# Kernel tuning notes

Measured on AMD Instinct MI355X. Metric: run time of the kernel, lower is better.

## Reference

```python
import jax, jax.numpy as jnp
import numpy as np

N_NODES = 50000
N_EDGES = 800000
N_GRAPHS = 256
F_IN = 112   # num_features
DIM = 32     # hidden dim of 2nd GIN layer
OUT_DIM = 64 # output_dim
BN_EPS = 1e-5


def setup_inputs() -> dict:
    key = jax.random.key(0)
    ks = jax.random.split(key, 20)
    def w(k, shape, s=0.05):
        return jax.random.normal(k, shape, dtype=jnp.float32) * s
    return {
        "x": jax.random.normal(ks[0], (N_NODES, F_IN), dtype=jnp.float32),
        "src": jax.random.randint(ks[1], (N_EDGES,), 0, N_NODES),
        "dst": jax.random.randint(ks[2], (N_EDGES,), 0, N_NODES),
        "batch": jnp.sort(jax.random.randint(ks[3], (N_NODES,), 0, N_GRAPHS)),
        # GIN layer 1 MLP: Linear(112,112) -> ReLU -> Linear(112,112)
        "g1_w1": w(ks[4], (F_IN, F_IN)), "g1_b1": jnp.zeros((F_IN,), jnp.float32),
        "g1_w2": w(ks[5], (F_IN, F_IN)), "g1_b2": jnp.zeros((F_IN,), jnp.float32),
        "bn1_g": jnp.ones((F_IN,), jnp.float32), "bn1_b": jnp.zeros((F_IN,), jnp.float32),
        # GIN layer 2 MLP: Linear(112,32) -> ReLU -> Linear(32,32)
        "g2_w1": w(ks[6], (F_IN, DIM)), "g2_b1": jnp.zeros((DIM,), jnp.float32),
        "g2_w2": w(ks[7], (DIM, DIM)), "g2_b2": jnp.zeros((DIM,), jnp.float32),
        "bn2_g": jnp.ones((DIM,), jnp.float32), "bn2_b": jnp.zeros((DIM,), jnp.float32),
        # graph-level head
        "fcxd_w": w(ks[8], (DIM, OUT_DIM)), "fcxd_b": jnp.zeros((OUT_DIM,), jnp.float32),
        "fc1_w": w(ks[9], (64, 32)), "fc1_b": jnp.zeros((32,), jnp.float32),
        "fc2_w": w(ks[10], (32, 16)), "fc2_b": jnp.zeros((16,), jnp.float32),
        "fc3_w": w(ks[11], (16, 8)), "fc3_b": jnp.zeros((8,), jnp.float32),
        "fc4_w": w(ks[12], (8, 2)), "fc4_b": jnp.zeros((2,), jnp.float32),
        "fc5_w": w(ks[13], (2, 1)), "fc5_b": jnp.zeros((1,), jnp.float32),
    }


def _batchnorm(h, g, b):
    # training-mode BatchNorm1d: batch statistics over node axis
    m = h.mean(axis=0)
    v = h.var(axis=0)
    return (h - m) * jax.lax.rsqrt(v + BN_EPS) * g + b


def reference(x, src, dst, batch,
              g1_w1, g1_b1, g1_w2, g1_b2, bn1_g, bn1_b,
              g2_w1, g2_b1, g2_w2, g2_b2, bn2_g, bn2_b,
              fcxd_w, fcxd_b, fc1_w, fc1_b, fc2_w, fc2_b,
              fc3_w, fc3_b, fc4_w, fc4_b, fc5_w, fc5_b):
    # --- GIN layer 1: agg = sum_{j in N(i)} x_j ; h = MLP(x + agg) (eps=0) ---
    agg = jax.ops.segment_sum(x[src], dst, num_segments=N_NODES)
    h = x + agg
    h = jnp.maximum(h @ g1_w1 + g1_b1, 0.0) @ g1_w2 + g1_b2
    h = jnp.maximum(h, 0.0)                     # F.relu after conv
    h = _batchnorm(h, bn1_g, bn1_b)
    # --- GIN layer 2 ---
    agg = jax.ops.segment_sum(h[src], dst, num_segments=N_NODES)
    h = h + agg
    h = jnp.maximum(h @ g2_w1 + g2_b1, 0.0) @ g2_w2 + g2_b2
    h = jnp.maximum(h, 0.0)
    h = _batchnorm(h, bn2_g, bn2_b)
    # --- global_add_pool over graph ids ---
    pooled = jax.ops.segment_sum(h, batch, num_segments=N_GRAPHS)  # [G, 32]
    z = jnp.maximum(pooled @ fcxd_w + fcxd_b, 0.0)  # dropout = identity (eval)
    # dense head: NO activations between fc1..fc5 in the original code
    z = z @ fc1_w + fc1_b
    z = z @ fc2_w + fc2_b
    z = z @ fc3_w + fc3_b
    z = z @ fc4_w + fc4_b
    z = z @ fc5_w + fc5_b
    return z  # [N_GRAPHS, 1]
```

## Files before the change

kernel.cpp:

```cpp
#include <hip/hip_runtime.h>
#include <hip/hip_fp16.h>

#define N_NODES 50000
#define N_GRAPHS 256
#define N_EDGES 800000
#define F_IN 112
#define DIM 32
#define BN_EPS 1e-5
#define HROW 128
#define CAP 64
#define CB 391
#define CBCAP 2560
#define CHUNK 8192
#define NPART 98
#define GEMM_MB 782
#define WS 40

typedef __attribute__((ext_vector_type(8))) _Float16 half8;
typedef __attribute__((ext_vector_type(4))) float float4v;

__device__ inline unsigned short f2h_u(float f) {
    union { __half h; unsigned short u; } v; v.h = __float2half(f); return v.u;
}
__device__ inline float h2f_u(unsigned short u) {
    union { unsigned short u; __half h; } v; v.u = u; return __half2float(v.h);
}

__device__ inline void acc8(const uint4& u, float* ax) {
    const __half2* h = (const __half2*)&u;
#pragma unroll
    for (int p = 0; p < 4; p++) {
        float2 f = __half22float2(h[p]);
        ax[2 * p] += f.x;
        ax[2 * p + 1] += f.y;
    }
}

__device__ inline void w_split_body(const float* __restrict__ W, int K, int N, int Kpad,
                                    unsigned short* __restrict__ hi_t,
                                    unsigned short* __restrict__ lo_t, int idx) {
    if (idx >= N * Kpad) return;
    int n = idx / Kpad, k = idx - n * Kpad;
    float v = (k < K) ? W[(size_t)k * N + n] : 0.f;
    unsigned short h = f2h_u(v);
    hi_t[idx] = h;
    lo_t[idx] = f2h_u(v - h2f_u(h));
}

#define MB_P  NPART
#define MB_XH (MB_P + 3126)
#define MB_W1 (MB_XH + 14)
#define MB_W2 (MB_W1 + 14)
#define MB_W4 (MB_W2 + 1)
#define MB_GB (MB_W4 + 49)
__global__ __launch_bounds__(1024) void build_kernel(
        const int* __restrict__ src, const int* __restrict__ dst,
        int* __restrict__ gcur,
        int* __restrict__ bucket,
        const float* __restrict__ X, __half* __restrict__ Xh,
        const float* __restrict__ g1_w1, unsigned short* w1h, unsigned short* w1l,
        const float* __restrict__ g1_w2, unsigned short* w2h, unsigned short* w2l,
        const float* __restrict__ g2_w2, unsigned short* w4h, unsigned short* w4l,
        const int* __restrict__ batch, int* __restrict__ goff) {
    int b = blockIdx.x;
    int t = threadIdx.x;
    if (b < MB_P) {
        __shared__ int hist[512];
        __shared__ int lofs[512];
        __shared__ int lcur[512];
        __shared__ int gbase[512];
        __shared__ int staging[CHUNK];
        int base = b * CHUNK;
        int total = min(CHUNK, N_EDGES - base);
        for (int i = t; i < 512; i += 1024) hist[i] = 0;
        __syncthreads();
        int d[8], s[8];
#pragma unroll
        for (int j = 0; j < 8; j++) {
            int i = base + j * 1024 + t;
            if (i < N_EDGES) {
                d[j] = __builtin_nontemporal_load(dst + i);
                s[j] = __builtin_nontemporal_load(src + i);
            } else {
                d[j] = -1;
            }
        }
#pragma unroll
        for (int j = 0; j < 8; j++) {
            if (d[j] >= 0) atomicAdd(&hist[d[j] >> 7], 1);
        }
        __syncthreads();
        if (t < 512) lofs[t] = hist[t];
        __syncthreads();
        for (int o = 1; o < 512; o <<= 1) {
            int add = (t < 512 && t >= o) ? lofs[t - o] : 0;
            __syncthreads();
            if (t < 512) lofs[t] += add;
            __syncthreads();
        }
        if (t < CB) {
            gbase[t] = (hist[t] > 0) ? atomicAdd(&gcur[t], hist[t]) : 0;
        }
        if (t < 512) lcur[t] = lofs[t] - hist[t];
        __syncthreads();
#pragma unroll
        for (int j = 0; j < 8; j++) {
            if (d[j] >= 0) {
                int bb = d[j] >> 7;
                int p = atomicAdd(&lcur[bb], 1);
                staging[p] = (d[j] << 16) | s[j];
            }
        }
        __syncthreads();
        for (int p = t; p < total; p += 1024) {
            int e = staging[p];
            int bb = ((unsigned)e >> 16) >> 7;
            int ls = lofs[bb] - hist[bb];
            int di = gbase[bb] + (p - ls);
            if (di < CBCAP) bucket[(size_t)bb * CBCAP + di] = e;
        }
    } else if (b < MB_XH) {
        int idx = (b - MB_P) * 1024 + t;
        if (idx >= (N_NODES + 1) * (HROW / 2)) return;
        int row = idx >> 6, c2 = idx & 63;
        int col = c2 * 2;
        float2 v = make_float2(0.f, 0.f);
        if (row < N_NODES && col < F_IN) v = *(const float2*)(X + (size_t)row * F_IN + col);
        ((__half2*)Xh)[idx] = __floats2half2_rn(v.x, v.y);
    } else if (b < MB_W1) {
        w_split_body(g1_w1, F_IN, F_IN, 128, w1h, w1l, (b - MB_XH) * 1024 + t);
    } else if (b < MB_W2) {
        w_split_body(g1_w2, F_IN, F_IN, 128, w2h, w2l, (b - MB_W1) * 1024 + t);
    } else if (b < MB_W4) {
        w_split_body(g2_w2, DIM, DIM, 32, w4h, w4l, (b - MB_W2) * 1024 + t);
    } else {
        int i = (b - MB_W4) * 1024 + t;
        if (i >= N_NODES) return;
        int cur = batch[i];
        int prev = (i == 0) ? -1 : batch[i - 1];
        for (int g = prev + 1; g <= cur; g++) goff[g] = i;
        if (i == N_NODES - 1) {
            for (int g = cur + 1; g <= N_GRAPHS; g++) goff[g] = N_NODES;
        }
    }
}

__global__ __launch_bounds__(1024) void bin_build(const int* __restrict__ gcur,
                                                  const int* __restrict__ bucket,
                                                  unsigned short* __restrict__ perm_pad,
                                                  int* __restrict__ deg) {
    __shared__ __align__(16) unsigned short bins[128][CAP];
    __shared__ int lcur[128];
    int b = blockIdx.x, t = threadIdx.x;
    for (int i = t; i < 128 * CAP; i += 1024) ((unsigned short*)bins)[i] = (unsigned short)N_NODES;
    if (t < 128) lcur[t] = 0;
    __syncthreads();
    int count = min(gcur[b], CBCAP);
    for (int i = t; i < count; i += 1024) {
        int e = bucket[(size_t)b * CBCAP + i];
        int l = ((unsigned)e >> 16) & 127;
        int s = e & 0xFFFF;
        int c = atomicAdd(&lcur[l], 1);
        if (c < CAP) bins[l][c] = (unsigned short)s;
    }
    __syncthreads();
    if (t < 128) {
        int node = b * 128 + t;
        if (node < N_NODES) deg[node] = min(lcur[t], CAP);
    }
    for (int i = t; i < 128 * (CAP / 8); i += 1024) {
        int l = i >> 3, q = i & 7;
        int node = b * 128 + l;
        if (node < N_NODES) {
            ((int4*)&perm_pad[(size_t)node * CAP])[q] = ((const int4*)bins[l])[q];
        }
    }
}

__global__ __launch_bounds__(1024, 8) void gin1_fused(const float* __restrict__ X,
        const __half* __restrict__ Xh,
        const int* __restrict__ deg_arr,
        const unsigned short* __restrict__ perm_pad,
        const unsigned short* __restrict__ W1h, const unsigned short* __restrict__ W1l,
        const float* __restrict__ b1,
        const unsigned short* __restrict__ W2h, const unsigned short* __restrict__ W2l,
        const float* __restrict__ b2,
        __half* __restrict__ Ch, float* __restrict__ pbuf, int M) {
    constexpr int N = 112, Kpad = 128, TS = 136, AS = 136;
    __shared__ __align__(16) unsigned short Afull[64 * AS];
    __shared__ __align__(16) unsigned short T1[64 * TS];
    __shared__ __align__(16) unsigned short Wh[N * WS];
    __shared__ __align__(16) unsigned short Wl[N * WS];
    float* sls = (float*)Afull;
    int t = threadIdx.x;
    int lane = t & 63, wid = t >> 6;
    int r0 = blockIdx.x * 64;
    int m = lane & 15, quad = lane >> 4;
    int rg = wid & 3, ng = wid >> 2;
    int nt0 = ng, nt1 = ng + 4;
    bool has1 = (nt1 < 7);

    for (int idx = t; idx < N * 8; idx += 1024) {
        int n = idx >> 3, w = idx & 7;
        int gsrc = n * (Kpad / 4) + w;
        ((uint2*)&Wh[n * WS])[w] = ((const uint2*)W1h)[gsrc];
        ((uint2*)&Wl[n * WS])[w] = ((const uint2*)W1l)[gsrc];
    }

    int fl = lane & 15, eg = lane >> 4;
#pragma unroll 1
    for (int i = 0; i < 4; i++) {
        int row = wid * 4 + i;
        int grow = r0 + row;
        float ax[8] = {0.f, 0.f, 0.f, 0.f, 0.f, 0.f, 0.f, 0.f};
        if (grow < M) {
            int deg = deg_arr[grow];
            const unsigned short* pl = perm_pad + (size_t)grow * CAP;
            int nb = (deg + 3) >> 2;
#pragma unroll 1
            for (int b = 0; b < nb; b += 4) {
                int s0 = pl[(b + 0) * 4 + eg];
                int s1 = pl[(b + 1) * 4 + eg];
                int s2 = pl[(b + 2) * 4 + eg];
                int s3 = pl[(b + 3) * 4 + eg];
                uint4 u0 = *(const uint4*)(Xh + (size_t)s0 * HROW + fl * 8);
                uint4 u1 = *(const uint4*)(Xh + (size_t)s1 * HROW + fl * 8);
                uint4 u2 = *(const uint4*)(Xh + (size_t)s2 * HROW + fl * 8);
                uint4 u3 = *(const uint4*)(Xh + (size_t)s3 * HROW + fl * 8);
                acc8(u0, ax); acc8(u1, ax); acc8(u2, ax); acc8(u3, ax);
            }
        }
#pragma unroll
        for (int p = 0; p < 8; p++) {
            ax[p] += __shfl_xor(ax[p], 16);
            ax[p] += __shfl_xor(ax[p], 32);
        }
        if (eg == 0) {
            if (grow < M && fl < 14) {
                float4 sa = *(const float4*)(X + (size_t)grow * F_IN + fl * 8);
                float4 sb = *(const float4*)(X + (size_t)grow * F_IN + fl * 8 + 4);
                ax[0] += sa.x; ax[1] += sa.y; ax[2] += sa.z; ax[3] += sa.w;
                ax[4] += sb.x; ax[5] += sb.y; ax[6] += sb.z; ax[7] += sb.w;
            }
            uint4 o;
            __half2* oh = (__half2*)&o;
#pragma unroll
            for (int p = 0; p < 4; p++) oh[p] = __floats2half2_rn(ax[2 * p], ax[2 * p + 1]);
            *(uint4*)&Afull[row * AS + fl * 8] = o;
        }
    }
    {
        int i = t;
        T1[(i >> 4) * TS + 112 + (i & 15)] = 0;
    }

    float4v acc0 = {0.f, 0.f, 0.f, 0.f}, acc1 = {0.f, 0.f, 0.f, 0.f};

    for (int c = 0; c < 4; c++) {
        int kc = c * 32;
        if (c > 0) {
            for (int idx = t; idx < N * 8; idx += 1024) {
                int n = idx >> 3, w = idx & 7;
                int gsrc = n * (Kpad / 4) + (kc >> 2) + w;
                ((uint2*)&Wh[n * WS])[w] = ((const uint2*)W1h)[gsrc];
                ((uint2*)&Wl[n * WS])[w] = ((const uint2*)W1l)[gsrc];
            }
        }
        __syncthreads();
        half8 a = *(const half8*)&Afull[(rg * 16 + m) * AS + kc + quad * 8];
        {
            half8 bh = *(const half8*)&Wh[(nt0 * 16 + m) * WS + quad * 8];
            half8 bl = *(const half8*)&Wl[(nt0 * 16 + m) * WS + quad * 8];
            acc0 = __builtin_amdgcn_mfma_f32_16x16x32_f16(a, bh, acc0, 0, 0, 0);
            acc0 = __builtin_amdgcn_mfma_f32_16x16x32_f16(a, bl, acc0, 0, 0, 0);
        }
        if (has1) {
            half8 bh = *(const half8*)&Wh[(nt1 * 16 + m) * WS + quad * 8];
            half8 bl = *(const half8*)&Wl[(nt1 * 16 + m) * WS + quad * 8];
            acc1 = __builtin_amdgcn_mfma_f32_16x16x32_f16(a, bh, acc1, 0, 0, 0);
            acc1 = __builtin_amdgcn_mfma_f32_16x16x32_f16(a, bl, acc1, 0, 0, 0);
        }
        __syncthreads();
    }

    {
        int col = nt0 * 16 + m;
        float bb = b1[col];
#pragma unroll
        for (int r = 0; r < 4; r++)
            T1[(rg * 16 + quad * 4 + r) * TS + col] = f2h_u(fmaxf(acc0[r] + bb, 0.f));
        acc0 = (float4v){0.f, 0.f, 0.f, 0.f};
    }
    if (has1) {
        int col = nt1 * 16 + m;
        float bb = b1[col];
#pragma unroll
        for (int r = 0; r < 4; r++)
            T1[(rg * 16 + quad * 4 + r) * TS + col] = f2h_u(fmaxf(acc1[r] + bb, 0.f));
        acc1 = (float4v){0.f, 0.f, 0.f, 0.f};
    }
    __syncthreads();

    for (int c = 0; c < 4; c++) {
        int kc = c * 32;
        for (int idx = t; idx < N * 8; idx += 1024) {
            int n = idx >> 3, w = idx & 7;
            int gsrc = n * (Kpad / 4) + (kc >> 2) + w;
            ((uint2*)&Wh[n * WS])[w] = ((const uint2*)W2h)[gsrc];
            ((uint2*)&Wl[n * WS])[w] = ((const uint2*)W2l)[gsrc];
        }
        __syncthreads();
        half8 a = *(const half8*)&T1[(rg * 16 + m) * TS + kc + quad * 8];
        {
            half8 bh = *(const half8*)&Wh[(nt0 * 16 + m) * WS + quad * 8];
            half8 bl = *(const half8*)&Wl[(nt0 * 16 + m) * WS + quad * 8];
            acc0 = __builtin_amdgcn_mfma_f32_16x16x32_f16(a, bh, acc0, 0, 0, 0);
            acc0 = __builtin_amdgcn_mfma_f32_16x16x32_f16(a, bl, acc0, 0, 0, 0);
        }
        if (has1) {
            half8 bh = *(const half8*)&Wh[(nt1 * 16 + m) * WS + quad * 8];
            half8 bl = *(const half8*)&Wl[(nt1 * 16 + m) * WS + quad * 8];
            acc1 = __builtin_amdgcn_mfma_f32_16x16x32_f16(a, bh, acc1, 0, 0, 0);
            acc1 = __builtin_amdgcn_mfma_f32_16x16x32_f16(a, bl, acc1, 0, 0, 0);
        }
        __syncthreads();
    }

    float st_s0 = 0.f, st_q0 = 0.f, st_s1 = 0.f, st_q1 = 0.f;
    {
        int col = nt0 * 16 + m;
        float bb = b2[col];
#pragma unroll
        for (int r = 0; r < 4; r++) {
            int row = r0 + rg * 16 + quad * 4 + r;
            float v = fmaxf(acc0[r] + bb, 0.f);
            if (row < M) {
                Ch[(size_t)row * HROW + col] = __float2half(v);
                st_s0 += v;
                st_q0 += v * v;
            }
        }
    }
    if (has1) {
        int col = nt1 * 16 + m;
        float bb = b2[col];
#pragma unroll
        for (int r = 0; r < 4; r++) {
            int row = r0 + rg * 16 + quad * 4 + r;
            float v = fmaxf(acc1[r] + bb, 0.f);
            if (row < M) {
                Ch[(size_t)row * HROW + col] = __float2half(v);
                st_s1 += v;
                st_q1 += v * v;
            }
        }
    }
    if (t < 128) {
        int row = r0 + (t >> 1), o = (t & 1) * 8;
        if (row < M) *(uint4*)((unsigned short*)Ch + (size_t)row * HROW + 112 + o) = make_uint4(0, 0, 0, 0);
    }
    st_s0 += __shfl_xor(st_s0, 16); st_s0 += __shfl_xor(st_s0, 32);
    st_q0 += __shfl_xor(st_q0, 16); st_q0 += __shfl_xor(st_q0, 32);
    st_s1 += __shfl_xor(st_s1, 16); st_s1 += __shfl_xor(st_s1, 32);
    st_q1 += __shfl_xor(st_q1, 16); st_q1 += __shfl_xor(st_q1, 32);
    if (quad == 0) {
        sls[rg * 2 * N + nt0 * 16 + m] = st_s0;
        sls[rg * 2 * N + N + nt0 * 16 + m] = st_q0;
        if (has1) {
            sls[rg * 2 * N + nt1 * 16 + m] = st_s1;
            sls[rg * 2 * N + N + nt1 * 16 + m] = st_q1;
        }
    }
    __syncthreads();
    if (t < 2 * N) {
        pbuf[(size_t)blockIdx.x * 2 * N + t] = sls[0 * 2 * N + t] + sls[1 * 2 * N + t] +
                                               sls[2 * 2 * N + t] + sls[3 * 2 * N + t];
    }
}

__global__ __launch_bounds__(256) void bn1_w3(const float* __restrict__ pbuf,
                                              const float* __restrict__ gg,
                                              const float* __restrict__ bb,
                                              const float* __restrict__ W,
                                              unsigned short* __restrict__ w3h,
                                              unsigned short* __restrict__ w3l,
                                              float* __restrict__ c0,
                                              __half* __restrict__ ysent, int M) {
    __shared__ double red[256];
    __shared__ float sv[2];
    int j = blockIdx.x;
    int t = threadIdx.x;
    if (j == 0 && t >= 64 && t < 96) ysent[t - 64] = __float2half(0.f);
    double sum = 0.0, sq = 0.0;
    for (int i = t; i < GEMM_MB; i += 256) {
        sum += (double)pbuf[(size_t)i * 2 * F_IN + j];
        sq  += (double)pbuf[(size_t)i * 2 * F_IN + F_IN + j];
    }
    red[t] = sum;
    __syncthreads();
    for (int o = 128; o > 0; o >>= 1) { if (t < o) red[t] += red[t + o]; __syncthreads(); }
    double total_sum = red[0];
    __syncthreads();
    red[t] = sq;
    __syncthreads();
    for (int o = 128; o > 0; o >>= 1) { if (t < o) red[t] += red[t + o]; __syncthreads(); }
    if (t == 0) {
        double mean = total_sum / M;
        double var = red[0] / M - mean * mean;
        double sc = (double)gg[j] / sqrt(var + BN_EPS);
        sv[0] = (float)sc;
        sv[1] = (float)((double)bb[j] - mean * sc);
    }
    __syncthreads();
    if (t < DIM) {
        float w = W[(size_t)j * DIM + t];
        float v = sv[0] * w;
        unsigned short h = f2h_u(v);
        w3h[t * 128 + j] = h;
        w3l[t * 128 + j] = f2h_u(v - h2f_u(h));
        atomicAdd(&c0[t], sv[1] * w);
    }
}

template <int NT, int KC, int ASG, int CHS>
__global__ __launch_bounds__(256) void gemm_mfma_h(const unsigned short* __restrict__ A,
                                                   const unsigned short* __restrict__ Whi,
                                                   const unsigned short* __restrict__ Wlo,
                                                   __half* __restrict__ Ch, int M) {
    constexpr int N = NT * 16;
    constexpr int Kpad = KC * 32;
    __shared__ __align__(16) unsigned short Ah[64 * WS];
    __shared__ __align__(16) unsigned short Wh[N * WS];
    __shared__ __align__(16) unsigned short Wl[N * WS];
    int t = threadIdx.x;
    int lane = t & 63, wid = t >> 6;
    int r0 = blockIdx.x * 64;
    int m = lane & 15, quad = lane >> 4;

    float4v acc[NT];
#pragma unroll
    for (int nt = 0; nt < NT; nt++) acc[nt] = (float4v){0.f, 0.f, 0.f, 0.f};

    for (int c = 0; c < KC; c++) {
        int kc = c * 32;
        {
            int row = t >> 2, seg = t & 3;
            int grow = r0 + row;
            uint4 v = make_uint4(0, 0, 0, 0);
            if (grow < M) v = *(const uint4*)(A + (size_t)grow * ASG + kc + seg * 8);
            *(uint4*)&Ah[row * WS + seg * 8] = v;
        }
        for (int idx = t; idx < N * 8; idx += 256) {
            int n = idx >> 3, w = idx & 7;
            int gsrc = n * (Kpad / 4) + (kc >> 2) + w;
            ((uint2*)&Wh[n * WS])[w] = ((const uint2*)Whi)[gsrc];
            ((uint2*)&Wl[n * WS])[w] = ((const uint2*)Wlo)[gsrc];
        }
        __syncthreads();
        half8 a = *(const half8*)&Ah[(wid * 16 + m) * WS + quad * 8];
#pragma unroll
        for (int nt = 0; nt < NT; nt++) {
            half8 b_h = *(const half8*)&Wh[(nt * 16 + m) * WS + quad * 8];
            half8 b_l = *(const half8*)&Wl[(nt * 16 + m) * WS + quad * 8];
            acc[nt] = __builtin_amdgcn_mfma_f32_16x16x32_f16(a, b_h, acc[nt], 0, 0, 0);
            acc[nt] = __builtin_amdgcn_mfma_f32_16x16x32_f16(a, b_l, acc[nt], 0, 0, 0);
        }
        __syncthreads();
    }
#pragma unroll
    for (int nt = 0; nt < NT; nt++) {
        int col = nt * 16 + m;
#pragma unroll
        for (int r = 0; r < 4; r++) {
            int row = r0 + wid * 16 + quad * 4 + r;
            if (row < M) Ch[(size_t)row * CHS + col] = __float2half(acc[nt][r]);
        }
    }
}

__global__ __launch_bounds__(512, 8) void gin2_fused(const __half* __restrict__ Y,
        const int* __restrict__ deg_arr,
        const unsigned short* __restrict__ perm_pad,
        const float* __restrict__ c0, const float* __restrict__ cb1,
        const unsigned short* __restrict__ W4h, const unsigned short* __restrict__ W4l,
        const float* __restrict__ bias,
        float* __restrict__ C, float* __restrict__ pbuf, int M) {
    constexpr int N = 32;
    __shared__ __align__(16) unsigned short As[64 * WS];
    __shared__ __align__(16) unsigned short Wh[N * WS];
    __shared__ __align__(16) unsigned short Wl[N * WS];
    __shared__ float sls[4][2 * N];
    int t = threadIdx.x;
    int lane = t & 63, wid = t >> 6;
    int r0 = blockIdx.x * 64;
    int m = lane & 15, quad = lane >> 4;
    int rg = wid & 3, nt = wid >> 2;

    for (int idx = t; idx < N * 8; idx += 512) {
        int n = idx >> 3, w = idx & 7;
        int gsrc = n * 8 + w;
        ((uint2*)&Wh[n * WS])[w] = ((const uint2*)W4h)[gsrc];
        ((uint2*)&Wl[n * WS])[w] = ((const uint2*)W4l)[gsrc];
    }

    int seg = lane & 3, eg = lane >> 2;
#pragma unroll 1
    for (int i = 0; i < 8; i++) {
        int row = wid * 8 + i;
        int grow = r0 + row;
        float ax[8] = {0.f, 0.f, 0.f, 0.f, 0.f, 0.f, 0.f, 0.f};
        int deg = 0;
        if (grow < M) {
            deg = deg_arr[grow];
            const unsigned short* pl = perm_pad + (size_t)grow * CAP;
            int nb = (deg + 15) >> 4;
#pragma unroll 1
            for (int b = 0; b < nb; b += 2) {
                int s0 = pl[(b + 0) * 16 + eg];
                int s1 = pl[(b + 1) * 16 + eg];
                uint4 u0 = *(const uint4*)(Y + (size_t)s0 * DIM + seg * 8);
                uint4 u1 = *(const uint4*)(Y + (size_t)s1 * DIM + seg * 8);
                acc8(u0, ax); acc8(u1, ax);
            }
        }
#pragma unroll
        for (int p = 0; p < 8; p++) {
            ax[p] += __shfl_xor(ax[p], 4);
            ax[p] += __shfl_xor(ax[p], 8);
            ax[p] += __shfl_xor(ax[p], 16);
            ax[p] += __shfl_xor(ax[p], 32);
        }
        if (eg == 0) {
            uint4 o = make_uint4(0, 0, 0, 0);
            if (grow < M) {
                uint4 sv = *(const uint4*)(Y + (size_t)grow * DIM + seg * 8);
                float deg1 = (float)(deg + 1);
                const __half2* sh = (const __half2*)&sv;
                __half2* oh = (__half2*)&o;
#pragma unroll
                for (int p = 0; p < 4; p++) {
                    float2 sf = __half22float2(sh[p]);
                    int f0 = seg * 8 + 2 * p;
                    float zx = fmaxf(sf.x + ax[2 * p] + deg1 * c0[f0] + cb1[f0], 0.f);
                    float zy = fmaxf(sf.y + ax[2 * p + 1] + deg1 * c0[f0 + 1] + cb1[f0 + 1], 0.f);
                    oh[p] = __floats2half2_rn(zx, zy);
                }
            }
            *(uint4*)&As[row * WS + seg * 8] = o;
        }
    }
    __syncthreads();

    float4v acc = {0.f, 0.f, 0.f, 0.f};
    half8 a = *(const half8*)&As[(rg * 16 + m) * WS + quad * 8];
    half8 bh = *(const half8*)&Wh[(nt * 16 + m) * WS + quad * 8];
    half8 bl = *(const half8*)&Wl[(nt * 16 + m) * WS + quad * 8];
    acc = __builtin_amdgcn_mfma_f32_16x16x32_f16(a, bh, acc, 0, 0, 0);
    acc = __builtin_amdgcn_mfma_f32_16x16x32_f16(a, bl, acc, 0, 0, 0);

    int col = nt * 16 + m;
    float b = bias[col];
    float s_loc = 0.f, q_loc = 0.f;
#pragma unroll
    for (int r = 0; r < 4; r++) {
        int row = r0 + rg * 16 + quad * 4 + r;
        float v = fmaxf(acc[r] + b, 0.f);
        if (row < M) {
            C[(size_t)row * N + col] = v;
            s_loc += v;
            q_loc += v * v;
        }
    }
    s_loc += __shfl_xor(s_loc, 16); s_loc += __shfl_xor(s_loc, 32);
    q_loc += __shfl_xor(q_loc, 16); q_loc += __shfl_xor(q_loc, 32);
    if (quad == 0) {
        sls[rg][col] = s_loc;
        sls[rg][N + col] = q_loc;
    }
    __syncthreads();
    if (t < 2 * N) {
        pbuf[(size_t)blockIdx.x * 2 * N + t] = sls[0][t] + sls[1][t] + sls[2][t] + sls[3][t];
    }
}

template <int F, int BLOCKS>
__global__ __launch_bounds__(256) void bn_finalize_par(const float* __restrict__ pbuf,
                                                       const float* __restrict__ g,
                                                       const float* __restrict__ b,
                                                       float* __restrict__ s,
                                                       float* __restrict__ tt, int M) {
    __shared__ double red[256];
    int j = blockIdx.x;
    int t = threadIdx.x;
    double sum = 0.0, sq = 0.0;
    for (int i = t; i < BLOCKS; i += 256) {
        sum += (double)pbuf[(size_t)i * 2 * F + j];
        sq  += (double)pbuf[(size_t)i * 2 * F + F + j];
    }
    red[t] = sum;
    __syncthreads();
    for (int o = 128; o > 0; o >>= 1) { if (t < o) red[t] += red[t + o]; __syncthreads(); }
    double total_sum = red[0];
    __syncthreads();
    red[t] = sq;
    __syncthreads();
    for (int o = 128; o > 0; o >>= 1) { if (t < o) red[t] += red[t + o]; __syncthreads(); }
    if (t == 0) {
        double mean = total_sum / M;
        double var = red[0] / M - mean * mean;
        double sc = (double)g[j] / sqrt(var + BN_EPS);
        s[j] = (float)sc;
        tt[j] = (float)((double)b[j] - mean * sc);
    }
}

__global__ __launch_bounds__(256) void pool_head(const float* __restrict__ H2, const int* __restrict__ goff,
                                                 const float* __restrict__ s2, const float* __restrict__ t2,
                                                 const float* __restrict__ fcxd_w, const float* __restrict__ fcxd_b,
                                                 const float* __restrict__ fc1_w, const float* __restrict__ fc1_b,
                                                 const float* __restrict__ fc2_w, const float* __restrict__ fc2_b,
                                                 const float* __restrict__ fc3_w, const float* __restrict__ fc3_b,
                                                 const float* __restrict__ fc4_w, const float* __restrict__ fc4_b,
                                                 const float* __restrict__ fc5_w, const float* __restrict__ fc5_b,
                                                 float* __restrict__ out) {
    __shared__ float red[256];
    __shared__ float p[64];
    __shared__ float z[64];
    int g = blockIdx.x, t = threadIdx.x;
    int r0 = goff[g], r1 = goff[g + 1];
    int cnt = r1 - r0;
    int j = t & 31, rr = t >> 5;
    float a = 0.f;
    for (int r = r0 + rr; r < r1; r += 8) a += H2[(size_t)r * DIM + j];
    red[t] = a;
    __syncthreads();
    if (t < 32) {
        float ssum = 0.f;
        for (int q = 0; q < 8; q++) ssum += red[q * 32 + j];
        p[j] = s2[j] * ssum + (float)cnt * t2[j];
    }
    __syncthreads();
    if (t < 64) {
        float acc = fcxd_b[t];
        for (int i = 0; i < 32; i++) acc += p[i] * fcxd_w[i * 64 + t];
        z[t] = fmaxf(acc, 0.f);
    }
    __syncthreads();
    if (t < 32) {
        float acc = fc1_b[t];
        for (int i = 0; i < 64; i++) acc += z[i] * fc1_w[i * 32 + t];
        p[t] = acc;
    }
    __syncthreads();
    if (t < 16) {
        float acc = fc2_b[t];
        for (int i = 0; i < 32; i++) acc += p[i] * fc2_w[i * 16 + t];
        z[t] = acc;
    }
    __syncthreads();
    if (t < 8) {
        float acc = fc3_b[t];
        for (int i = 0; i < 16; i++) acc += z[i] * fc3_w[i * 8 + t];
        p[t] = acc;
    }
    __syncthreads();
    if (t < 2) {
        float acc = fc4_b[t];
        for (int i = 0; i < 8; i++) acc += p[i] * fc4_w[i * 2 + t];
        z[t] = acc;
    }
    __syncthreads();
    if (t == 0) {
        out[g] = z[0] * fc5_w[0] + z[1] * fc5_w[1] + fc5_b[0];
    }
}

extern "C" void kernel_launch(void* const* d_in, const int* in_sizes, int n_in,
                              void* d_out, int out_size, void* d_ws, size_t ws_size,
                              hipStream_t stream) {
    const float* x     = (const float*)d_in[0];
    const int*   src   = (const int*)d_in[1];
    const int*   dst   = (const int*)d_in[2];
    const int*   batch = (const int*)d_in[3];
    const float* g1_w1 = (const float*)d_in[4];
    const float* g1_b1 = (const float*)d_in[5];
    const float* g1_w2 = (const float*)d_in[6];
    const float* g1_b2 = (const float*)d_in[7];
    const float* bn1_g = (const float*)d_in[8];
    const float* bn1_b = (const float*)d_in[9];
    const float* g2_w1 = (const float*)d_in[10];
    const float* g2_b1 = (const float*)d_in[11];
    const float* g2_w2 = (const float*)d_in[12];
    const float* g2_b2 = (const float*)d_in[13];
    const float* bn2_g = (const float*)d_in[14];
    const float* bn2_b = (const float*)d_in[15];
    const float* fcxd_w = (const float*)d_in[16];
    const float* fcxd_b = (const float*)d_in[17];
    const float* fc1_w = (const float*)d_in[18];
    const float* fc1_b = (const float*)d_in[19];
    const float* fc2_w = (const float*)d_in[20];
    const float* fc2_b = (const float*)d_in[21];
    const float* fc3_w = (const float*)d_in[22];
    const float* fc3_b = (const float*)d_in[23];
    const float* fc4_w = (const float*)d_in[24];
    const float* fc4_b = (const float*)d_in[25];
    const float* fc5_w = (const float*)d_in[26];
    const float* fc5_b = (const float*)d_in[27];
    float* out = (float*)d_out;
    char* ws = (char*)d_ws;

    size_t off = 0;
    auto take = [&](size_t bytes) { size_t o = off; off += (bytes + 255) & ~(size_t)255; return o; };
    int* gcur      = (int*)(ws + take((size_t)CB * 4));
    float* c0      = (float*)(ws + take(DIM * 4));
    unsigned short* w3h = (unsigned short*)(ws + take((size_t)DIM * 128 * 2));
    unsigned short* w3l = (unsigned short*)(ws + take((size_t)DIM * 128 * 2));
    size_t zero_bytes = off;
    int* bucket    = (int*)(ws + take((size_t)CB * CBCAP * 4));
    unsigned short* perm_pad = (unsigned short*)(ws + take((size_t)N_NODES * CAP * 2));
    int* deg       = (int*)(ws + take((size_t)N_NODES * 4));
    int* goff      = (int*)(ws + take((size_t)(N_GRAPHS + 4) * 4));
    float* s2      = (float*)(ws + take(DIM * 4));
    float* t2      = (float*)(ws + take(DIM * 4));
    float* pb1     = (float*)(ws + take((size_t)GEMM_MB * 2 * F_IN * 4));
    float* pb2     = (float*)(ws + take((size_t)GEMM_MB * 2 * DIM * 4));
    unsigned short* w1h = (unsigned short*)(ws + take((size_t)F_IN * 128 * 2));
    unsigned short* w1l = (unsigned short*)(ws + take((size_t)F_IN * 128 * 2));
    unsigned short* w2h = (unsigned short*)(ws + take((size_t)F_IN * 128 * 2));
    unsigned short* w2l = (unsigned short*)(ws + take((size_t)F_IN * 128 * 2));
    unsigned short* w4h = (unsigned short*)(ws + take((size_t)DIM * 32 * 2));
    unsigned short* w4l = (unsigned short*)(ws + take((size_t)DIM * 32 * 2));
    __half* x_half = (__half*)(ws + take((size_t)(N_NODES + 1) * HROW * 2));
    __half* h1h    = (__half*)(ws + take((size_t)N_NODES * HROW * 2));
    __half* y_half = (__half*)(ws + take((size_t)(N_NODES + 1) * DIM * 2));
    float* bufS2   = (float*)(ws + take((size_t)N_NODES * DIM * 4));
    (void)ws_size; (void)in_sizes; (void)n_in; (void)out_size;

    hipMemsetAsync(ws, 0, zero_bytes, stream);

    build_kernel<<<MB_GB, 1024, 0, stream>>>(src, dst, gcur, bucket,
                                             x, x_half,
                                             g1_w1, w1h, w1l, g1_w2, w2h, w2l, g2_w2, w4h, w4l,
                                             batch, goff);
    bin_build<<<CB, 1024, 0, stream>>>(gcur, bucket, perm_pad, deg);

    gin1_fused<<<GEMM_MB, 1024, 0, stream>>>(x, x_half, deg, perm_pad,
                                             w1h, w1l, g1_b1, w2h, w2l, g1_b2,
                                             h1h, pb1, N_NODES);
    bn1_w3<<<F_IN, 256, 0, stream>>>(pb1, bn1_g, bn1_b, g2_w1, w3h, w3l, c0,
                                     y_half + (size_t)N_NODES * DIM, N_NODES);

    gemm_mfma_h<2, 4, HROW, DIM><<<GEMM_MB, 256, 0, stream>>>(
        (const unsigned short*)h1h, w3h, w3l, y_half, N_NODES);
    gin2_fused<<<GEMM_MB, 512, 0, stream>>>(y_half, deg, perm_pad, c0, g2_b1,
                                            w4h, w4l, g2_b2, bufS2, pb2, N_NODES);
    bn_finalize_par<DIM, GEMM_MB><<<DIM, 256, 0, stream>>>(pb2, bn2_g, bn2_b, s2, t2, N_NODES);

    pool_head<<<N_GRAPHS, 256, 0, stream>>>(bufS2, goff, s2, t2,
                                            fcxd_w, fcxd_b, fc1_w, fc1_b, fc2_w, fc2_b,
                                            fc3_w, fc3_b, fc4_w, fc4_b, fc5_w, fc5_b, out);
}
```

Measured before the change: 241.1 us.

## Fuse neighbor bin building into GIN aggregation kernels, drop bin_build pass

Removes the separate bin_build kernel and the perm_pad/deg global arrays. Each gin1/gin2 block now rebuilds its 64 rows' neighbor lists in shared memory from the bucketed edges, using sentinel padding so gathers can run fixed-width unrolled batches (8 in gin1, a fixed 4 in gin2). This trades a kernel launch and global write/read traffic for duplicated bucket scans (done twice, once per layer) and extra LDS use that may reduce occupancy.

```diff
diff --git a/kernel.cpp b/kernel.cpp
--- a/kernel.cpp
+++ b/kernel.cpp
@@ -15,6 +15,7 @@
 #define NPART 98
 #define GEMM_MB 782
 #define WS 40
+#define SENT2 0xC350C350u
 
 typedef __attribute__((ext_vector_type(8))) _Float16 half8;
 typedef __attribute__((ext_vector_type(4))) float float4v;
@@ -145,42 +146,10 @@
     }
 }
 
-__global__ __launch_bounds__(1024) void bin_build(const int* __restrict__ gcur,
-                                                  const int* __restrict__ bucket,
-                                                  unsigned short* __restrict__ perm_pad,
-                                                  int* __restrict__ deg) {
-    __shared__ __align__(16) unsigned short bins[128][CAP];
-    __shared__ int lcur[128];
-    int b = blockIdx.x, t = threadIdx.x;
-    for (int i = t; i < 128 * CAP; i += 1024) ((unsigned short*)bins)[i] = (unsigned short)N_NODES;
-    if (t < 128) lcur[t] = 0;
-    __syncthreads();
-    int count = min(gcur[b], CBCAP);
-    for (int i = t; i < count; i += 1024) {
-        int e = bucket[(size_t)b * CBCAP + i];
-        int l = ((unsigned)e >> 16) & 127;
-        int s = e & 0xFFFF;
-        int c = atomicAdd(&lcur[l], 1);
-        if (c < CAP) bins[l][c] = (unsigned short)s;
-    }
-    __syncthreads();
-    if (t < 128) {
-        int node = b * 128 + t;
-        if (node < N_NODES) deg[node] = min(lcur[t], CAP);
-    }
-    for (int i = t; i < 128 * (CAP / 8); i += 1024) {
-        int l = i >> 3, q = i & 7;
-        int node = b * 128 + l;
-        if (node < N_NODES) {
-            ((int4*)&perm_pad[(size_t)node * CAP])[q] = ((const int4*)bins[l])[q];
-        }
-    }
-}
-
 __global__ __launch_bounds__(1024, 8) void gin1_fused(const float* __restrict__ X,
         const __half* __restrict__ Xh,
-        const int* __restrict__ deg_arr,
-        const unsigned short* __restrict__ perm_pad,
+        const int* __restrict__ gcur,
+        const int* __restrict__ bucket,
         const unsigned short* __restrict__ W1h, const unsigned short* __restrict__ W1l,
         const float* __restrict__ b1,
         const unsigned short* __restrict__ W2h, const unsigned short* __restrict__ W2l,
@@ -191,6 +160,8 @@
     __shared__ __align__(16) unsigned short T1[64 * TS];
     __shared__ __align__(16) unsigned short Wh[N * WS];
     __shared__ __align__(16) unsigned short Wl[N * WS];
+    __shared__ __align__(16) unsigned short bins[64][CAP];
+    __shared__ int lcur[64];
     float* sls = (float*)Afull;
     int t = threadIdx.x;
     int lane = t & 63, wid = t >> 6;
@@ -200,35 +171,50 @@
     int nt0 = ng, nt1 = ng + 4;
     bool has1 = (nt1 < 7);
 
+    for (int i = t; i < 64 * CAP / 2; i += 1024) ((unsigned int*)bins)[i] = SENT2;
+    if (t < 64) lcur[t] = 0;
+
     for (int idx = t; idx < N * 8; idx += 1024) {
         int n = idx >> 3, w = idx & 7;
         int gsrc = n * (Kpad / 4) + w;
         ((uint2*)&Wh[n * WS])[w] = ((const uint2*)W1h)[gsrc];
         ((uint2*)&Wl[n * WS])[w] = ((const uint2*)W1l)[gsrc];
     }
+    __syncthreads();
+
+    {
+        int cb = blockIdx.x >> 1, half = blockIdx.x & 1;
+        int count = min(gcur[cb], CBCAP);
+        for (int i = t; i < count; i += 1024) {
+            int e = bucket[(size_t)cb * CBCAP + i];
+            int l = ((unsigned)e >> 16) & 127;
+            if ((l >> 6) == half) {
+                int c = atomicAdd(&lcur[l & 63], 1);
+                if (c < CAP) bins[l & 63][c] = (unsigned short)(e & 0xFFFF);
+            }
+        }
+    }
+    __syncthreads();
 
     int fl = lane & 15, eg = lane >> 4;
 #pragma unroll 1
     for (int i = 0; i < 4; i++) {
         int row = wid * 4 + i;
         int grow = r0 + row;
+        int deg = min(lcur[row], CAP);
         float ax[8] = {0.f, 0.f, 0.f, 0.f, 0.f, 0.f, 0.f, 0.f};
-        if (grow < M) {
-            int deg = deg_arr[grow];
-            const unsigned short* pl = perm_pad + (size_t)grow * CAP;
-            int nb = (deg + 3) >> 2;
+        const unsigned short* pl = bins[row];
+        int nb = (deg + 3) >> 2;
 #pragma unroll 1
-            for (int b = 0; b < nb; b += 4) {
-                int s0 = pl[(b + 0) * 4 + eg];
-                int s1 = pl[(b + 1) * 4 + eg];
-                int s2 = pl[(b + 2) * 4 + eg];
-                int s3 = pl[(b + 3) * 4 + eg];
-                uint4 u0 = *(const uint4*)(Xh + (size_t)s0 * HROW + fl * 8);
-                uint4 u1 = *(const uint4*)(Xh + (size_t)s1 * HROW + fl * 8);
-                uint4 u2 = *(const uint4*)(Xh + (size_t)s2 * HROW + fl * 8);
-                uint4 u3 = *(const uint4*)(Xh + (size_t)s3 * HROW + fl * 8);
-                acc8(u0, ax); acc8(u1, ax); acc8(u2, ax); acc8(u3, ax);
-            }
+        for (int b = 0; b < nb; b += 8) {
+            int s[8];
+#pragma unroll
+            for (int j = 0; j < 8; j++) s[j] = pl[(b + j) * 4 + eg];
+            uint4 u[8];
+#pragma unroll
+            for (int j = 0; j < 8; j++) u[j] = *(const uint4*)(Xh + (size_t)s[j] * HROW + fl * 8);
+#pragma unroll
+            for (int j = 0; j < 8; j++) acc8(u[j], ax);
         }
 #pragma unroll
         for (int p = 0; p < 8; p++) {
@@ -479,8 +465,8 @@
 }
 
 __global__ __launch_bounds__(512, 8) void gin2_fused(const __half* __restrict__ Y,
-        const int* __restrict__ deg_arr,
-        const unsigned short* __restrict__ perm_pad,
+        const int* __restrict__ gcur,
+        const int* __restrict__ bucket,
         const float* __restrict__ c0, const float* __restrict__ cb1,
         const unsigned short* __restrict__ W4h, const unsigned short* __restrict__ W4l,
         const float* __restrict__ bias,
@@ -489,6 +475,8 @@
     __shared__ __align__(16) unsigned short As[64 * WS];
     __shared__ __align__(16) unsigned short Wh[N * WS];
     __shared__ __align__(16) unsigned short Wl[N * WS];
+    __shared__ __align__(16) unsigned short bins[64][CAP];
+    __shared__ int lcur[64];
     __shared__ float sls[4][2 * N];
     int t = threadIdx.x;
     int lane = t & 63, wid = t >> 6;
@@ -496,32 +484,48 @@
     int m = lane & 15, quad = lane >> 4;
     int rg = wid & 3, nt = wid >> 2;
 
+    for (int i = t; i < 64 * CAP / 2; i += 512) ((unsigned int*)bins)[i] = SENT2;
+    if (t < 64) lcur[t] = 0;
+
     for (int idx = t; idx < N * 8; idx += 512) {
         int n = idx >> 3, w = idx & 7;
         int gsrc = n * 8 + w;
         ((uint2*)&Wh[n * WS])[w] = ((const uint2*)W4h)[gsrc];
         ((uint2*)&Wl[n * WS])[w] = ((const uint2*)W4l)[gsrc];
     }
+    __syncthreads();
+
+    {
+        int cb = blockIdx.x >> 1, half = blockIdx.x & 1;
+        int count = min(gcur[cb], CBCAP);
+        for (int i = t; i < count; i += 512) {
+            int e = bucket[(size_t)cb * CBCAP + i];
+            int l = ((unsigned)e >> 16) & 127;
+            if ((l >> 6) == half) {
+                int c = atomicAdd(&lcur[l & 63], 1);
+                if (c < CAP) bins[l & 63][c] = (unsigned short)(e & 0xFFFF);
+            }
+        }
+    }
+    __syncthreads();
 
     int seg = lane & 3, eg = lane >> 2;
 #pragma unroll 1
     for (int i = 0; i < 8; i++) {
         int row = wid * 8 + i;
         int grow = r0 + row;
+        int deg = min(lcur[row], CAP);
         float ax[8] = {0.f, 0.f, 0.f, 0.f, 0.f, 0.f, 0.f, 0.f};
-        int deg = 0;
         if (grow < M) {
-            deg = deg_arr[grow];
-            const unsigned short* pl = perm_pad + (size_t)grow * CAP;
-            int nb = (deg + 15) >> 4;
-#pragma unroll 1
-            for (int b = 0; b < nb; b += 2) {
-                int s0 = pl[(b + 0) * 16 + eg];
-                int s1 = pl[(b + 1) * 16 + eg];
-                uint4 u0 = *(const uint4*)(Y + (size_t)s0 * DIM + seg * 8);
-                uint4 u1 = *(const uint4*)(Y + (size_t)s1 * DIM + seg * 8);
-                acc8(u0, ax); acc8(u1, ax);
-            }
+            const unsigned short* pl = bins[row];
+            int s[4];
+#pragma unroll
+            for (int j = 0; j < 4; j++) s[j] = pl[j * 16 + eg];
+            uint4 u[4];
+#pragma unroll
+            for (int j = 0; j < 4; j++) u[j] = *(const uint4*)(Y + (size_t)s[j] * DIM + seg * 8);
+#pragma unroll
+            for (int j = 0; j < 4; j++) acc8(u[j], ax);
         }
 #pragma unroll
         for (int p = 0; p < 8; p++) {
@@ -717,8 +721,6 @@
     unsigned short* w3l = (unsigned short*)(ws + take((size_t)DIM * 128 * 2));
     size_t zero_bytes = off;
     int* bucket    = (int*)(ws + take((size_t)CB * CBCAP * 4));
-    unsigned short* perm_pad = (unsigned short*)(ws + take((size_t)N_NODES * CAP * 2));
-    int* deg       = (int*)(ws + take((size_t)N_NODES * 4));
     int* goff      = (int*)(ws + take((size_t)(N_GRAPHS + 4) * 4));
     float* s2      = (float*)(ws + take(DIM * 4));
     float* t2      = (float*)(ws + take(DIM * 4));
@@ -742,9 +744,8 @@
                                              x, x_half,
                                              g1_w1, w1h, w1l, g1_w2, w2h, w2l, g2_w2, w4h, w4l,
                                              batch, goff);
-    bin_build<<<CB, 1024, 0, stream>>>(gcur, bucket, perm_pad, deg);
-
-    gin1_fused<<<GEMM_MB, 1024, 0, stream>>>(x, x_half, deg, perm_pad,
+
+    gin1_fused<<<GEMM_MB, 1024, 0, stream>>>(x, x_half, gcur, bucket,
                                              w1h, w1l, g1_b1, w2h, w2l, g1_b2,
                                              h1h, pb1, N_NODES);
     bn1_w3<<<F_IN, 256, 0, stream>>>(pb1, bn1_g, bn1_b, g2_w1, w3h, w3l, c0,
@@ -752,7 +753,7 @@
 
     gemm_mfma_h<2, 4, HROW, DIM><<<GEMM_MB, 256, 0, stream>>>(
         (const unsigned short*)h1h, w3h, w3l, y_half, N_NODES);
-    gin2_fused<<<GEMM_MB, 512, 0, stream>>>(y_half, deg, perm_pad, c0, g2_b1,
+    gin2_fused<<<GEMM_MB, 512, 0, stream>>>(y_half, gcur, bucket, c0, g2_b1,
                                             w4h, w4l, g2_b2, bufS2, pb2, N_NODES);
     bn_finalize_par<DIM, GEMM_MB><<<DIM, 256, 0, stream>>>(pb2, bn2_g, bn2_b, s2, t2, N_NODES);
 
```

Result: slower. 323.6 us (+34.2%).
